# Kernel optimization log

Hardware: AMD Instinct MI355X
Metric: run time of the kernel (lower is better)

The kernel has to match this reference:

```python
import jax, jax.numpy as jnp
import numpy as np

B, N, C = 8, 3136, 128
NUM_HEADS = 2
HEAD_DIM = C // NUM_HEADS  # 64
SCALE = HEAD_DIM ** -0.5


def setup_inputs() -> dict:
    key = jax.random.key(0)
    ks = jax.random.split(key, 10)
    s = 0.02
    return {
        "x": jax.random.normal(ks[0], (B, N, C), jnp.float32),
        "H": 56,
        "W": 56,
        "relative_pos": jax.random.normal(ks[1], (NUM_HEADS, N, N), jnp.float32),
        "Wq": jax.random.normal(ks[2], (C, C), jnp.float32) * s,
        "bq": jnp.zeros((C,), jnp.float32),
        "Wk": jax.random.normal(ks[3], (C, C), jnp.float32) * s,
        "bk": jnp.zeros((C,), jnp.float32),
        "Wv": jax.random.normal(ks[4], (C, C), jnp.float32) * s,
        "bv": jnp.zeros((C,), jnp.float32),
        "Wp": jax.random.normal(ks[5], (C, C), jnp.float32) * s,
        "bp": jnp.zeros((C,), jnp.float32),
    }


def reference(x, H, W, relative_pos, Wq, bq, Wk, bk, Wv, bv, Wp, bp):
    # x: [B, N, C]; sr_ratio == 1 path of Attention.forward
    b, n, c = x.shape
    h, dh = NUM_HEADS, HEAD_DIM
    # q/k/v projections -> [B, h, N, dh] (torch Linear: x @ W.T + b)
    q = (x @ Wq.T + bq).reshape(b, n, h, dh).transpose(0, 2, 1, 3)
    k = (x @ Wk.T + bk).reshape(b, n, h, dh).transpose(0, 2, 1, 3)
    v = (x @ Wv.T + bv).reshape(b, n, h, dh).transpose(0, 2, 1, 3)
    # scores with additive relative-position bias: [B, h, N, N]
    attn = jnp.einsum("bhnd,bhmd->bhnm", q, k) * SCALE + relative_pos[None]
    attn = jax.nn.softmax(attn, axis=-1)
    # AV -> [B, N, C]
    out = jnp.einsum("bhnm,bhmd->bhnd", attn, v).transpose(0, 2, 1, 3).reshape(b, n, c)
    return out @ Wp.T + bp
```

## Files before the change

kernel.cpp:

```cpp
#include <hip/hip_runtime.h>
#include <hip/hip_fp16.h>

#define N_TOK 3136
#define DH 64
#define NHEAD 2
#define CDIM 128
#define BATCH 8
#define NT 49
#define QT1 49
#define MTILES ((BATCH * N_TOK) / 64)
#define EXPBLKS (NHEAD * NT * (N_TOK / 64))
#define QK_SCALE 0.18033688011112f
#define LOG2E 1.4426950408889634f

typedef __attribute__((ext_vector_type(8))) short bf16x8;
typedef __attribute__((ext_vector_type(8))) _Float16 f16x8;
typedef __attribute__((ext_vector_type(2))) _Float16 f16x2;
typedef __attribute__((ext_vector_type(2))) __fp16 fp16x2;
typedef __attribute__((ext_vector_type(4))) float f32x4;
typedef __attribute__((ext_vector_type(16))) float f32x16;
typedef __attribute__((ext_vector_type(4))) unsigned short u16x4;
typedef __attribute__((ext_vector_type(4))) unsigned int u32x4;

__device__ __forceinline__ unsigned short f2bf(float f) {
  unsigned int u = __float_as_uint(f);
  u += 0x7fffu + ((u >> 16) & 1u);
  return (unsigned short)(u >> 16);
}

#define MFMA16(a, b, c)    __builtin_amdgcn_mfma_f32_16x16x32_bf16(a, b, c, 0, 0, 0)
#define MFMA32_BF(a, b, c) __builtin_amdgcn_mfma_f32_32x32x16_bf16(a, b, c, 0, 0, 0)
#define MFMA32_F16(a, b, c) __builtin_amdgcn_mfma_f32_32x32x16_f16(a, b, c, 0, 0, 0)

__device__ __forceinline__ void plswap(unsigned& a, unsigned& b) {
  asm volatile("v_permlane32_swap_b32 %0, %1" : "+v"(a), "+v"(b));
}

__device__ __forceinline__ f16x2 pkrtz(float a, float b) {
  union { fp16x2 p; f16x2 h; } cv;
  cv.p = __builtin_amdgcn_cvt_pkrtz(a, b);
  return cv.h;
}

__device__ __forceinline__ float dot2acc(f16x2 pr, float acc) {
#if __has_builtin(__builtin_amdgcn_fdot2)
  union { f16x2 h; fp16x2 p; } c; c.h = pr;
  fp16x2 ones = {(__fp16)1.0f, (__fp16)1.0f};
  return __builtin_amdgcn_fdot2(c.p, ones, acc, false);
#else
  return acc + (float)pr[0] + (float)pr[1];
#endif
}

__device__ __forceinline__ void stage_w(const float* __restrict__ W,
                                        unsigned short (*wsh)[136], int tid) {
  const float4* Wv4 = (const float4*)W;
#pragma unroll
  for (int i = 0; i < 16; ++i) {
    int f = tid + i * 256;
    float4 v = Wv4[f];
    int row = f >> 5, col = (f & 31) << 2;
    u16x4 pk = { f2bf(v.x), f2bf(v.y), f2bf(v.z), f2bf(v.w) };
    *(u16x4*)&wsh[row][col] = pk;
  }
}

__device__ __forceinline__ void mfma_block(const unsigned short (*xs)[136],
                                           const unsigned short (*wsh)[136],
                                           int w, int lk, int lg, f32x4* acc) {
#pragma unroll
  for (int nf = 0; nf < 8; ++nf) acc[nf] = (f32x4){0.f, 0.f, 0.f, 0.f};
#pragma unroll
  for (int kk = 0; kk < 4; ++kk) {
    bf16x8 a = *(const bf16x8*)&xs[w * 16 + lk][kk * 32 + 8 * lg];
#pragma unroll
    for (int nf = 0; nf < 8; ++nf) {
      bf16x8 b = *(const bf16x8*)&wsh[nf * 16 + lk][kk * 32 + 8 * lg];
      acc[nf] = MFMA16(a, b, acc[nf]);
    }
  }
}

__global__ __launch_bounds__(256)
void pre_kernel(const float* __restrict__ x,
                const float* __restrict__ Wq, const float* __restrict__ bq,
                const float* __restrict__ Wk, const float* __restrict__ bk,
                const float* __restrict__ Wv, const float* __restrict__ bv,
                unsigned short* __restrict__ qo, unsigned short* __restrict__ ko,
                unsigned short* __restrict__ vo,
                const float* __restrict__ rp, __half* __restrict__ E)
{
  __shared__ __align__(16) unsigned short xs[64][136];
  __shared__ __align__(16) unsigned short wsh[128][136];
  const int tid = threadIdx.x;

  if (blockIdx.x >= MTILES) {
    const int eb = blockIdx.x - MTILES;
    const int hkt = eb % (NHEAD * NT);
    const int q0 = (eb / (NHEAD * NT)) * 64;
    const int h = hkt / NT, kt = hkt % NT;
    const int kp = tid & 63;
    const int qi = tid >> 6;

    const int ct = kp >> 5;
    const int kpp = kp & 31;
    const int hi = (kpp >> 2) & 1;
    const int r = (kpp & 3) + ((kpp >> 3) << 2);
    const int didx = hi * 32 + ct * 16 + r;

    const float* src = rp + ((size_t)h * N_TOK + q0) * N_TOK + kt * 64 + kp;
    __half* dst = E + (((size_t)h * NT + kt) * N_TOK + q0) * 64 + didx;
#pragma unroll
    for (int i = 0; i < 16; ++i) {
      int q = qi * 16 + i;
      float v = __expf(src[(size_t)q * N_TOK]);
      dst[(size_t)q * 64] = __float2half(v);
    }
    return;
  }

  const int m0 = blockIdx.x * 64;
  const int w = tid >> 6, l = tid & 63;
  const int lk = l & 15, lg = l >> 4;

  {
    const float4* Xv = (const float4*)(x + (size_t)m0 * CDIM);
#pragma unroll
    for (int i = 0; i < 8; ++i) {
      int f = tid + i * 256;
      float4 v = Xv[f];
      int row = f >> 5, col = (f & 31) << 2;
      u16x4 pk = { f2bf(v.x), f2bf(v.y), f2bf(v.z), f2bf(v.w) };
      *(u16x4*)&xs[row][col] = pk;
    }
  }
  stage_w(Wq, wsh, tid);
  __syncthreads();

  f32x4 acc[8];

  mfma_block(xs, wsh, w, lk, lg, acc);
#pragma unroll
  for (int reg = 0; reg < 4; ++reg) {
    int row = m0 + w * 16 + 4 * lg + reg;
    int bb = row / N_TOK, tok = row - bb * N_TOK;
#pragma unroll
    for (int nf = 0; nf < 8; ++nf) {
      int col = nf * 16 + lk;
      float val = (acc[nf][reg] + bq[col]) * QK_SCALE;
      qo[((size_t)(bb * NHEAD + (nf >> 2)) * N_TOK + tok) * DH + (col & 63)] = f2bf(val);
    }
  }
  __syncthreads();

  stage_w(Wk, wsh, tid);
  __syncthreads();
  mfma_block(xs, wsh, w, lk, lg, acc);
#pragma unroll
  for (int reg = 0; reg < 4; ++reg) {
    int row = m0 + w * 16 + 4 * lg + reg;
    int bb = row / N_TOK, tok = row - bb * N_TOK;
#pragma unroll
    for (int nf = 0; nf < 8; ++nf) {
      int col = nf * 16 + lk;
      float val = acc[nf][reg] + bk[col];
      ko[((size_t)(bb * NHEAD + (nf >> 2)) * N_TOK + tok) * DH + (col & 63)] = f2bf(val);
    }
  }
  __syncthreads();

  stage_w(Wv, wsh, tid);
  __syncthreads();
  mfma_block(xs, wsh, w, lk, lg, acc);
#pragma unroll
  for (int reg = 0; reg < 4; ++reg) {
    int row = m0 + w * 16 + 4 * lg + reg;
    int bb = row / N_TOK, tok = row - bb * N_TOK;
#pragma unroll
    for (int nf = 0; nf < 8; ++nf) {
      int col = nf * 16 + lk;
      float val = acc[nf][reg] + bv[col];
      size_t idx = ((size_t)(bb * NHEAD + (nf >> 2)) * DH + (col & 63)) * N_TOK + tok;
      vo[idx] = __half_as_ushort(__float2half(val));
    }
  }
}

__global__ __launch_bounds__(128)
void attn32(const unsigned short* __restrict__ q_ws,
            const unsigned short* __restrict__ k_ws,
            const unsigned short* __restrict__ v_ws,
            const __half* __restrict__ E,
            unsigned short* __restrict__ attn_out)
{
  __shared__ __align__(16) unsigned short LDSU[2][9216];

  const int b = blockIdx.x, qt = blockIdx.y, head = blockIdx.z;
  const int tid = threadIdx.x;
  const int w = tid >> 6, l = tid & 63;
  const int lq = l & 31, hi = l >> 5;

  const size_t bh = ((size_t)b * NHEAD + head) * N_TOK;
  const unsigned short* Kp = k_ws + bh * DH;
  const _Float16* Vt = (const _Float16*)v_ws + bh * DH;

  const int qg = qt * 64 + w * 32 + lq;

  bf16x8 qf[4];
  {
    const unsigned short* qrow = q_ws + (bh + (size_t)qg) * DH + 8 * hi;
#pragma unroll
    for (int ks = 0; ks < 4; ++ks) qf[ks] = *(const bf16x8*)(qrow + 16 * ks);
  }

  const int sr = tid >> 3, su = tid & 7;
  const int kofs = sr * 72 + su * 8;
  const int gk = sr * DH + su * 8;
  const int gvt = sr * N_TOK + su * 8;

  const __half* Eb = E + (((size_t)head * NT) * N_TOK + (size_t)qg) * DH + hi * 32;

  float lsum = 0.f;
  f32x16 o0, o1;
#pragma unroll
  for (int i = 0; i < 16; ++i) { o0[i] = 0.f; o1[i] = 0.f; }

  bf16x8 kpre[4]; f16x8 vpre[4];
#pragma unroll
  for (int i = 0; i < 4; ++i) {
    kpre[i] = *(const bf16x8*)(Kp + gk + i * 16 * DH);
    vpre[i] = *(const f16x8*)(Vt + gvt + i * 16 * N_TOK);
  }

  u32x4 EwA[4], EwB[4];
  {
    const u32x4* ep = (const u32x4*)Eb;
#pragma unroll
    for (int f = 0; f < 4; ++f) EwA[f] = ep[f];
  }

#pragma unroll
  for (int i = 0; i < 4; ++i) {
    *(bf16x8*)&LDSU[0][kofs + i * 1152] = kpre[i];
    *(f16x8*)&LDSU[0][4608 + kofs + i * 1152] = vpre[i];
  }
  {
    const unsigned short* kn = Kp + (size_t)64 * DH;
    const _Float16* vn = Vt + 64;
#pragma unroll
    for (int i = 0; i < 4; ++i) {
      kpre[i] = *(const bf16x8*)(kn + gk + i * 16 * DH);
      vpre[i] = *(const f16x8*)(vn + gvt + i * 16 * N_TOK);
    }
  }
  asm volatile("s_waitcnt lgkmcnt(0)" ::: "memory");
  __builtin_amdgcn_s_barrier();
  asm volatile("" ::: "memory");

#define ATTN_BODY(PH, KT, EW_CUR, EW_NXT)                                     \
  {                                                                           \
    const bool hasNext = (KT) + 1 < NT;                                       \
    const unsigned short* Kb = &LDSU[PH][0];                                  \
    const unsigned short* Vb = &LDSU[PH][4608];                               \
    unsigned short* Kn = &LDSU[PH ^ 1][0];                                    \
    unsigned short* Vn = &LDSU[PH ^ 1][4608];                                 \
    if (hasNext) {                                         \
      const u32x4* ep = (const u32x4*)(Eb + (size_t)((KT) + 1) * (N_TOK * DH)); \
      _Pragma("unroll") for (int f = 0; f < 4; ++f) EW_NXT[f] = ep[f];        \
    }                                                                         \
                                                           \
    f32x16 s0, s1;                                                            \
    _Pragma("unroll") for (int i = 0; i < 16; ++i) { s0[i] = 0.f; s1[i] = 0.f; } \
    __builtin_amdgcn_s_setprio(1);                                            \
    _Pragma("unroll") for (int ks = 0; ks < 4; ++ks) {                        \
      bf16x8 kf0 = *(const bf16x8*)&Kb[lq * 72 + 16 * ks + 8 * hi];           \
      s0 = MFMA32_BF(kf0, qf[ks], s0);                                        \
      bf16x8 kf1 = *(const bf16x8*)&Kb[(32 + lq) * 72 + 16 * ks + 8 * hi];    \
      s1 = MFMA32_BF(kf1, qf[ks], s1);                                        \
    }                                                                         \
    __builtin_amdgcn_s_setprio(0);                                            \
    if (hasNext) {            \
      _Pragma("unroll") for (int i = 0; i < 4; ++i) {                         \
        *(bf16x8*)&Kn[kofs + i * 1152] = kpre[i];                             \
        *(f16x8*)&Vn[kofs + i * 1152] = vpre[i];                              \
      }                                                                       \
      if ((KT) + 2 < NT) {                                                    \
        const unsigned short* kn2 = Kp + (size_t)((KT) + 2) * 64 * DH;        \
        const _Float16* vn2 = Vt + (size_t)((KT) + 2) * 64;                   \
        _Pragma("unroll") for (int i = 0; i < 4; ++i) {                       \
          kpre[i] = *(const bf16x8*)(kn2 + gk + i * 16 * DH);                 \
          vpre[i] = *(const f16x8*)(vn2 + gvt + i * 16 * N_TOK);              \
        }                                                                     \
      }                                                                       \
    }                                                                         \
                                \
    unsigned pw[16];                                                          \
    _Pragma("unroll") for (int f = 0; f < 4; ++f) {                           \
      int rb = (f & 1) * 8;                                                   \
      _Pragma("unroll") for (int i = 0; i < 4; ++i) {                         \
        float a = (f >> 1) ? s1[rb + 2 * i] : s0[rb + 2 * i];                 \
        float c = (f >> 1) ? s1[rb + 2 * i + 1] : s0[rb + 2 * i + 1];         \
        f16x2 pp = pkrtz(__builtin_amdgcn_exp2f(a), __builtin_amdgcn_exp2f(c)); \
        union { unsigned u; f16x2 h; } ec; ec.u = EW_CUR[f][i];               \
        f16x2 pr = pp * ec.h;                                                 \
        lsum = dot2acc(pr, lsum);                                             \
        union { f16x2 h; unsigned u; } pu; pu.h = pr;                         \
        pw[4 * f + i] = pu.u;                                                 \
      }                                                                       \
      plswap(pw[4 * f + 0], pw[4 * f + 2]);                                   \
      plswap(pw[4 * f + 1], pw[4 * f + 3]);                                   \
    }                                                                         \
                                                        \
    __builtin_amdgcn_s_setprio(1);                                            \
    _Pragma("unroll") for (int ks = 0; ks < 4; ++ks) {                        \
      union { unsigned u[4]; f16x8 v; } pf;                                   \
      _Pragma("unroll") for (int i = 0; i < 4; ++i) pf.u[i] = pw[4 * ks + i]; \
      f16x8 vf0 = *(const f16x8*)&Vb[lq * 72 + 16 * ks + 8 * hi];             \
      o0 = MFMA32_F16(vf0, pf.v, o0);                                         \
      f16x8 vf1 = *(const f16x8*)&Vb[(32 + lq) * 72 + 16 * ks + 8 * hi];      \
      o1 = MFMA32_F16(vf1, pf.v, o1);                                         \
    }                                                                         \
    __builtin_amdgcn_s_setprio(0);                                            \
    if (hasNext) {                                                            \
      asm volatile("s_waitcnt lgkmcnt(0)" ::: "memory");                      \
      __builtin_amdgcn_s_barrier();                                           \
      asm volatile("" ::: "memory");                                          \
    }                                                                         \
  }

  for (int kt2 = 0; kt2 < (NT - 1) / 2; ++kt2) {
    int kt = 2 * kt2;
    ATTN_BODY(0, kt, EwA, EwB);
    ATTN_BODY(1, kt + 1, EwB, EwA);
  }
  ATTN_BODY(0, NT - 1, EwA, EwB);
#undef ATTN_BODY

  lsum += __shfl_xor(lsum, 32, 64);
  float inv = 1.f / lsum;

  __syncthreads();
  unsigned short* Ot = &LDSU[0][0];
  const int orow = (w * 32 + lq) * 72;
#pragma unroll
  for (int dt = 0; dt < 2; ++dt) {
#pragma unroll
    for (int j = 0; j < 8; ++j) {
      float v0 = (dt ? o1[2 * j] : o0[2 * j]) * inv;
      float v1 = (dt ? o1[2 * j + 1] : o0[2 * j + 1]) * inv;
      unsigned pk;
      asm("v_cvt_pk_bf16_f32 %0, %1, %2" : "=v"(pk) : "v"(v0), "v"(v1));
      int d = ((2 * j) & 3) + 8 * ((2 * j) >> 2) + 4 * hi + 32 * dt;
      *(unsigned*)&Ot[orow + d] = pk;
    }
  }
  __syncthreads();
#pragma unroll
  for (int i = 0; i < 4; ++i) {
    int c = tid + 128 * i;
    int ql = c >> 3, du = c & 7;
    int tok = qt * 64 + ql;
    u32x4 val = *(const u32x4*)&Ot[ql * 72 + du * 8];
    *(u32x4*)&attn_out[((size_t)b * N_TOK + tok) * CDIM + head * DH + du * 8] = val;
  }
}

template<bool IN_F32, int OMODE>
__global__ __launch_bounds__(256)
void proj_gemm(const void* __restrict__ Ain, const float* __restrict__ W,
               const float* __restrict__ bias, void* __restrict__ Out,
               float out_scale)
{
  __shared__ __align__(16) unsigned short xs[64][136];
  __shared__ __align__(16) unsigned short wsh[128][136];
  const int tid = threadIdx.x;
  const int m0 = blockIdx.x * 64;
  const int w = tid >> 6, l = tid & 63;
  const int lk = l & 15, lg = l >> 4;

  stage_w(W, wsh, tid);
  if (IN_F32) {
    const float4* Xv = (const float4*)((const float*)Ain + (size_t)m0 * CDIM);
#pragma unroll
    for (int i = 0; i < 8; ++i) {
      int f = tid + i * 256;
      float4 v = Xv[f];
      int row = f >> 5, col = (f & 31) << 2;
      u16x4 pk = { f2bf(v.x), f2bf(v.y), f2bf(v.z), f2bf(v.w) };
      *(u16x4*)&xs[row][col] = pk;
    }
  } else {
    const bf16x8* Xv = (const bf16x8*)((const unsigned short*)Ain + (size_t)m0 * CDIM);
#pragma unroll
    for (int i = 0; i < 4; ++i) {
      int c = tid + i * 256;
      bf16x8 v = Xv[c];
      int row = c >> 4, col = (c & 15) << 3;
      *(bf16x8*)&xs[row][col] = v;
    }
  }
  __syncthreads();

  f32x4 acc[8];
  mfma_block(xs, wsh, w, lk, lg, acc);

#pragma unroll
  for (int reg = 0; reg < 4; ++reg) {
    int row = m0 + w * 16 + 4 * lg + reg;
    int bb = row / N_TOK;
    int tok = row - bb * N_TOK;
#pragma unroll
    for (int nf = 0; nf < 8; ++nf) {
      int col = nf * 16 + lk;
      float val = (acc[nf][reg] + bias[col]) * out_scale;
      if (OMODE == 0) {
        ((float*)Out)[(size_t)row * CDIM + col] = val;
      } else {
        int head = nf >> 2;
        int d = col & 63;
        size_t idx = ((size_t)(bb * NHEAD + head) * N_TOK + tok) * DH + d;
        ((unsigned short*)Out)[idx] = f2bf(val);
      }
    }
  }
}

__global__ __launch_bounds__(256)
void attn_fallback(const unsigned short* __restrict__ q_ws,
                   const unsigned short* __restrict__ k_ws,
                   const unsigned short* __restrict__ v_ws,
                   const float* __restrict__ relpos,
                   unsigned short* __restrict__ attn_out)
{
  __shared__ __align__(16) unsigned short Ks[64][72];
  __shared__ __align__(16) unsigned short Vts[64][72];
  __shared__ __align__(16) unsigned short Ps[4][16][72];

  const int b = blockIdx.x, qt = blockIdx.y, head = blockIdx.z;
  const int tid = threadIdx.x;
  const int w = tid >> 6, l = tid & 63;
  const int lk = l & 15, lg = l >> 4;

  const size_t bh = ((size_t)b * NHEAD + head) * N_TOK;
  const unsigned short* Qp = q_ws + (bh + (size_t)qt * 64) * DH;
  const unsigned short* Kp = k_ws + bh * DH;
  const unsigned short* Vg = v_ws + bh * DH;

  bf16x8 qf0, qf1;
  {
    const unsigned short* qrow = Qp + (size_t)(w * 16 + lk) * DH + 8 * lg;
    qf0 = *(const bf16x8*)qrow;
    qf1 = *(const bf16x8*)(qrow + 32);
  }

  const int kr0 = tid >> 3;
  const int ku = (tid & 7) << 3;
  const int gk0 = kr0 * DH + ku;
  const int gk1 = gk0 + 32 * DH;
  const int vkey = tid & 63;
  const int vd0 = (tid >> 6) << 3;
  const int gv0 = vkey * DH + vd0;
  const int gv1 = gv0 + 32;

  const int qrow0 = qt * 64 + w * 16;
  const float* rpb = relpos + (size_t)head * N_TOK * N_TOK +
                     (size_t)(qrow0 + 4 * lg) * N_TOK + lk;

  float l_run[4] = {0.f, 0.f, 0.f, 0.f};
  f32x4 acc[4];
#pragma unroll
  for (int nf = 0; nf < 4; ++nf) acc[nf] = (f32x4){0.f, 0.f, 0.f, 0.f};

  bf16x8 kpreA = *(const bf16x8*)(Kp + gk0);
  bf16x8 kpreB = *(const bf16x8*)(Kp + gk1);
  bf16x8 vpreA = *(const bf16x8*)(Vg + gv0);
  bf16x8 vpreB = *(const bf16x8*)(Vg + gv1);

  for (int kt = 0; kt < NT; ++kt) {
    float rp[4][4];
#pragma unroll
    for (int r = 0; r < 4; ++r)
#pragma unroll
      for (int ct = 0; ct < 4; ++ct)
        rp[ct][r] = rpb[(size_t)r * N_TOK + kt * 64 + ct * 16];

    asm volatile("s_waitcnt lgkmcnt(0)" ::: "memory");
    __builtin_amdgcn_s_barrier();
    asm volatile("" ::: "memory");

    *(bf16x8*)&Ks[kr0][ku] = kpreA;
    *(bf16x8*)&Ks[kr0 + 32][ku] = kpreB;
#pragma unroll
    for (int j = 0; j < 8; ++j) Vts[vd0 + j][vkey] = ((const unsigned short*)&vpreA)[j];
#pragma unroll
    for (int j = 0; j < 8; ++j) Vts[vd0 + 32 + j][vkey] = ((const unsigned short*)&vpreB)[j];

    if (kt + 1 < NT) {
      const unsigned short* kn = Kp + (size_t)(kt + 1) * 64 * DH;
      const unsigned short* vn = Vg + (size_t)(kt + 1) * 64 * DH;
      kpreA = *(const bf16x8*)(kn + gk0);
      kpreB = *(const bf16x8*)(kn + gk1);
      vpreA = *(const bf16x8*)(vn + gv0);
      vpreB = *(const bf16x8*)(vn + gv1);
    }

    asm volatile("s_waitcnt lgkmcnt(0)" ::: "memory");
    __builtin_amdgcn_s_barrier();
    asm volatile("" ::: "memory");

    f32x4 s[4];
#pragma unroll
    for (int ct = 0; ct < 4; ++ct) s[ct] = (f32x4){0.f, 0.f, 0.f, 0.f};
#pragma unroll
    for (int ct = 0; ct < 4; ++ct) {
      bf16x8 kb0 = *(const bf16x8*)&Ks[ct * 16 + lk][8 * lg];
      s[ct] = MFMA16(qf0, kb0, s[ct]);
      bf16x8 kb1 = *(const bf16x8*)&Ks[ct * 16 + lk][32 + 8 * lg];
      s[ct] = MFMA16(qf1, kb1, s[ct]);
    }

#pragma unroll
    for (int ct = 0; ct < 4; ++ct) {
      float p0 = __builtin_amdgcn_exp2f(fmaf(rp[ct][0], LOG2E, s[ct][0]));
      float p1 = __builtin_amdgcn_exp2f(fmaf(rp[ct][1], LOG2E, s[ct][1]));
      float p2 = __builtin_amdgcn_exp2f(fmaf(rp[ct][2], LOG2E, s[ct][2]));
      float p3 = __builtin_amdgcn_exp2f(fmaf(rp[ct][3], LOG2E, s[ct][3]));
      l_run[0] += p0; l_run[1] += p1; l_run[2] += p2; l_run[3] += p3;
      Ps[w][4 * lg + 0][ct * 16 + lk] = f2bf(p0);
      Ps[w][4 * lg + 1][ct * 16 + lk] = f2bf(p1);
      Ps[w][4 * lg + 2][ct * 16 + lk] = f2bf(p2);
      Ps[w][4 * lg + 3][ct * 16 + lk] = f2bf(p3);
    }

    bf16x8 pa0 = *(const bf16x8*)&Ps[w][lk][8 * lg];
    bf16x8 pa1 = *(const bf16x8*)&Ps[w][lk][32 + 8 * lg];
#pragma unroll
    for (int nf = 0; nf < 4; ++nf) {
      bf16x8 vb0 = *(const bf16x8*)&Vts[nf * 16 + lk][8 * lg];
      acc[nf] = MFMA16(pa0, vb0, acc[nf]);
      bf16x8 vb1 = *(const bf16x8*)&Vts[nf * 16 + lk][32 + 8 * lg];
      acc[nf] = MFMA16(pa1, vb1, acc[nf]);
    }
  }

#pragma unroll
  for (int m = 1; m <= 8; m <<= 1)
#pragma unroll
    for (int r = 0; r < 4; ++r)
      l_run[r] += __shfl_xor(l_run[r], m, 64);

#pragma unroll
  for (int r = 0; r < 4; ++r) {
    int tok = qrow0 + 4 * lg + r;
    float inv = 1.f / l_run[r];
#pragma unroll
    for (int nf = 0; nf < 4; ++nf) {
      attn_out[((size_t)b * N_TOK + tok) * CDIM + head * DH + nf * 16 + lk] =
          f2bf(acc[nf][r] * inv);
    }
  }
}

extern "C" void kernel_launch(void* const* d_in, const int* in_sizes, int n_in,
                              void* d_out, int out_size, void* d_ws, size_t ws_size,
                              hipStream_t stream) {
  (void)in_sizes; (void)n_in; (void)out_size;
  const float* x      = (const float*)d_in[0];
  const float* relpos = (const float*)d_in[3];
  const float* Wq = (const float*)d_in[4];  const float* bq = (const float*)d_in[5];
  const float* Wk = (const float*)d_in[6];  const float* bk = (const float*)d_in[7];
  const float* Wv = (const float*)d_in[8];  const float* bv = (const float*)d_in[9];
  const float* Wp = (const float*)d_in[10]; const float* bp = (const float*)d_in[11];

  const size_t QKV_ELEMS = (size_t)BATCH * NHEAD * N_TOK * DH;
  const size_t E_ELEMS   = (size_t)NHEAD * NT * N_TOK * DH;

  unsigned short* q_ws  = (unsigned short*)d_ws;
  unsigned short* k_ws  = q_ws + QKV_ELEMS;
  unsigned short* v_ws  = k_ws + QKV_ELEMS;
  unsigned short* ao_ws = v_ws + QKV_ELEMS;
  __half* E_ws = (__half*)(ao_ws + QKV_ELEMS);

  const size_t need_mid = (4 * QKV_ELEMS + E_ELEMS) * sizeof(unsigned short);

  dim3 blk(256);

  if (ws_size >= need_mid) {
    pre_kernel<<<MTILES + EXPBLKS, blk, 0, stream>>>(
        x, Wq, bq, Wk, bk, Wv, bv, q_ws, k_ws, v_ws, relpos, (__half*)E_ws);
    attn32<<<dim3(BATCH, QT1, NHEAD), dim3(128), 0, stream>>>(
        q_ws, k_ws, v_ws, (const __half*)E_ws, ao_ws);
  } else {
    proj_gemm<true, 1><<<MTILES, blk, 0, stream>>>((const void*)x, Wq, bq, (void*)q_ws, QK_SCALE);
    proj_gemm<true, 1><<<MTILES, blk, 0, stream>>>((const void*)x, Wk, bk, (void*)k_ws, 1.f);
    proj_gemm<true, 1><<<MTILES, blk, 0, stream>>>((const void*)x, Wv, bv, (void*)v_ws, 1.f);
    attn_fallback<<<dim3(BATCH, N_TOK / 64, NHEAD), blk, 0, stream>>>(
        q_ws, k_ws, v_ws, relpos, ao_ws);
  }

  proj_gemm<false, 0><<<MTILES, blk, 0, stream>>>((const void*)ao_ws, Wp, bp, d_out, 1.f);
}
```

Before: 117.9 us.

## Widen attention blocks to 128 queries and software-pipeline QK^T ahead of softmax

```diff
diff --git a/kernel.cpp b/kernel.cpp
--- a/kernel.cpp
+++ b/kernel.cpp
@@ -7,7 +7,6 @@
 #define CDIM 128
 #define BATCH 8
 #define NT 49
-#define QT1 49
 #define MTILES ((BATCH * N_TOK) / 64)
 #define EXPBLKS (NHEAD * NT * (N_TOK / 64))
 #define QK_SCALE 0.18033688011112f
@@ -186,14 +185,17 @@
   }
 }
 
-__global__ __launch_bounds__(128)
+__global__ __launch_bounds__(256)
 void attn32(const unsigned short* __restrict__ q_ws,
             const unsigned short* __restrict__ k_ws,
             const unsigned short* __restrict__ v_ws,
             const __half* __restrict__ E,
             unsigned short* __restrict__ attn_out)
 {
-  __shared__ __align__(16) unsigned short LDSU[2][9216];
+  __shared__ __align__(16) unsigned short LDSU[27648];
+
+#define KBUF(i) (&LDSU[(i) * 4608])
+#define VBUF(i) (&LDSU[9216 + (i) * 4608])
 
   const int b = blockIdx.x, qt = blockIdx.y, head = blockIdx.z;
   const int tid = threadIdx.x;
@@ -204,7 +206,8 @@
   const unsigned short* Kp = k_ws + bh * DH;
   const _Float16* Vt = (const _Float16*)v_ws + bh * DH;
 
-  const int qg = qt * 64 + w * 32 + lq;
+  int qg = qt * 128 + w * 32 + lq;
+  if (qg > N_TOK - 1) qg = N_TOK - 1;
 
   bf16x8 qf[4];
   {
@@ -215,132 +218,172 @@
 
   const int sr = tid >> 3, su = tid & 7;
   const int kofs = sr * 72 + su * 8;
-  const int gk = sr * DH + su * 8;
-  const int gvt = sr * N_TOK + su * 8;
+  const int gk0 = sr * DH + su * 8, gk1 = gk0 + 32 * DH;
+  const int gvt0 = sr * N_TOK + su * 8, gvt1 = gvt0 + 32 * N_TOK;
 
   const __half* Eb = E + (((size_t)head * NT) * N_TOK + (size_t)qg) * DH + hi * 32;
 
-  float lsum = 0.f;
-  f32x16 o0, o1;
+  float lsum0 = 0.f, lsum1 = 0.f;
+  f32x16 o0, o1, sA0, sA1, sB0, sB1;
 #pragma unroll
   for (int i = 0; i < 16; ++i) { o0[i] = 0.f; o1[i] = 0.f; }
 
-  bf16x8 kpre[4]; f16x8 vpre[4];
-#pragma unroll
-  for (int i = 0; i < 4; ++i) {
-    kpre[i] = *(const bf16x8*)(Kp + gk + i * 16 * DH);
-    vpre[i] = *(const f16x8*)(Vt + gvt + i * 16 * N_TOK);
-  }
+  bf16x8 kpreA = *(const bf16x8*)(Kp + gk0);
+  bf16x8 kpreB = *(const bf16x8*)(Kp + gk1);
+  f16x8 vpreA = *(const f16x8*)(Vt + gvt0);
+  f16x8 vpreB = *(const f16x8*)(Vt + gvt1);
 
   u32x4 EwA[4], EwB[4];
   {
     const u32x4* ep = (const u32x4*)Eb;
 #pragma unroll
     for (int f = 0; f < 4; ++f) EwA[f] = ep[f];
-  }
-
-#pragma unroll
-  for (int i = 0; i < 4; ++i) {
-    *(bf16x8*)&LDSU[0][kofs + i * 1152] = kpre[i];
-    *(f16x8*)&LDSU[0][4608 + kofs + i * 1152] = vpre[i];
-  }
+    const u32x4* ep1 = (const u32x4*)(Eb + (size_t)(N_TOK * DH));
+#pragma unroll
+    for (int f = 0; f < 4; ++f) EwB[f] = ep1[f];
+  }
+
+  *(bf16x8*)&KBUF(0)[kofs] = kpreA;
+  *(bf16x8*)&KBUF(0)[kofs + 32 * 72] = kpreB;
+  *(f16x8*)&VBUF(0)[kofs] = vpreA;
+  *(f16x8*)&VBUF(0)[kofs + 32 * 72] = vpreB;
   {
     const unsigned short* kn = Kp + (size_t)64 * DH;
     const _Float16* vn = Vt + 64;
-#pragma unroll
-    for (int i = 0; i < 4; ++i) {
-      kpre[i] = *(const bf16x8*)(kn + gk + i * 16 * DH);
-      vpre[i] = *(const f16x8*)(vn + gvt + i * 16 * N_TOK);
-    }
+    kpreA = *(const bf16x8*)(kn + gk0);
+    kpreB = *(const bf16x8*)(kn + gk1);
+    vpreA = *(const f16x8*)(vn + gvt0);
+    vpreB = *(const f16x8*)(vn + gvt1);
   }
   asm volatile("s_waitcnt lgkmcnt(0)" ::: "memory");
   __builtin_amdgcn_s_barrier();
   asm volatile("" ::: "memory");
 
-#define ATTN_BODY(PH, KT, EW_CUR, EW_NXT)                                     \
+#pragma unroll
+  for (int i = 0; i < 16; ++i) { sA0[i] = 0.f; sA1[i] = 0.f; }
+  __builtin_amdgcn_s_setprio(1);
+#pragma unroll
+  for (int ks = 0; ks < 4; ++ks) {
+    bf16x8 kf0 = *(const bf16x8*)&KBUF(0)[lq * 72 + 16 * ks + 8 * hi];
+    sA0 = MFMA32_BF(kf0, qf[ks], sA0);
+    bf16x8 kf1 = *(const bf16x8*)&KBUF(0)[(32 + lq) * 72 + 16 * ks + 8 * hi];
+    sA1 = MFMA32_BF(kf1, qf[ks], sA1);
+  }
+  __builtin_amdgcn_s_setprio(0);
+  *(bf16x8*)&KBUF(1)[kofs] = kpreA;
+  *(bf16x8*)&KBUF(1)[kofs + 32 * 72] = kpreB;
+  *(f16x8*)&VBUF(1)[kofs] = vpreA;
+  *(f16x8*)&VBUF(1)[kofs + 32 * 72] = vpreB;
+  {
+    const unsigned short* kn = Kp + (size_t)2 * 64 * DH;
+    const _Float16* vn = Vt + 2 * 64;
+    kpreA = *(const bf16x8*)(kn + gk0);
+    kpreB = *(const bf16x8*)(kn + gk1);
+    vpreA = *(const f16x8*)(vn + gvt0);
+    vpreB = *(const f16x8*)(vn + gvt1);
+  }
+  asm volatile("s_waitcnt lgkmcnt(0)" ::: "memory");
+  __builtin_amdgcn_s_barrier();
+  asm volatile("" ::: "memory");
+
+#define SOFTMAX(S0, S1, EW, PW, LSUM)                                         \
+    _Pragma("unroll") for (int f = 0; f < 4; ++f) {                           \
+      int rb = (f & 1) * 8;                                                   \
+      _Pragma("unroll") for (int i = 0; i < 4; ++i) {                         \
+        float a = (f >> 1) ? S1[rb + 2 * i] : S0[rb + 2 * i];                 \
+        float c = (f >> 1) ? S1[rb + 2 * i + 1] : S0[rb + 2 * i + 1];         \
+        f16x2 pp = pkrtz(__builtin_amdgcn_exp2f(a), __builtin_amdgcn_exp2f(c)); \
+        union { unsigned u; f16x2 h; } ec; ec.u = EW[f][i];                   \
+        f16x2 pr = pp * ec.h;                                                 \
+        LSUM = dot2acc(pr, LSUM);                                             \
+        union { f16x2 h; unsigned u; } pu; pu.h = pr;                         \
+        PW[4 * f + i] = pu.u;                                                 \
+      }                                                                       \
+      plswap(PW[4 * f + 0], PW[4 * f + 2]);                                   \
+      plswap(PW[4 * f + 1], PW[4 * f + 3]);                                   \
+    }
+
+#define BODY(KT, KC, KN, VP, VS, EWC, EWN, SC0, SC1, SP0, SP1, LSUM)          \
   {                                                                           \
-    const bool hasNext = (KT) + 1 < NT;                                       \
-    const unsigned short* Kb = &LDSU[PH][0];                                  \
-    const unsigned short* Vb = &LDSU[PH][4608];                               \
-    unsigned short* Kn = &LDSU[PH ^ 1][0];                                    \
-    unsigned short* Vn = &LDSU[PH ^ 1][4608];                                 \
-    if (hasNext) {                                         \
-      const u32x4* ep = (const u32x4*)(Eb + (size_t)((KT) + 1) * (N_TOK * DH)); \
-      _Pragma("unroll") for (int f = 0; f < 4; ++f) EW_NXT[f] = ep[f];        \
-    }                                                                         \
-                                                           \
-    f32x16 s0, s1;                                                            \
-    _Pragma("unroll") for (int i = 0; i < 16; ++i) { s0[i] = 0.f; s1[i] = 0.f; } \
+                      \
+    _Pragma("unroll") for (int i = 0; i < 16; ++i) { SC0[i] = 0.f; SC1[i] = 0.f; } \
     __builtin_amdgcn_s_setprio(1);                                            \
     _Pragma("unroll") for (int ks = 0; ks < 4; ++ks) {                        \
-      bf16x8 kf0 = *(const bf16x8*)&Kb[lq * 72 + 16 * ks + 8 * hi];           \
-      s0 = MFMA32_BF(kf0, qf[ks], s0);                                        \
-      bf16x8 kf1 = *(const bf16x8*)&Kb[(32 + lq) * 72 + 16 * ks + 8 * hi];    \
-      s1 = MFMA32_BF(kf1, qf[ks], s1);                                        \
+      bf16x8 kf0 = *(const bf16x8*)&(KC)[lq * 72 + 16 * ks + 8 * hi];         \
+      SC0 = MFMA32_BF(kf0, qf[ks], SC0);                                      \
+      bf16x8 kf1 = *(const bf16x8*)&(KC)[(32 + lq) * 72 + 16 * ks + 8 * hi];  \
+      SC1 = MFMA32_BF(kf1, qf[ks], SC1);                                      \
     }                                                                         \
     __builtin_amdgcn_s_setprio(0);                                            \
-    if (hasNext) {            \
-      _Pragma("unroll") for (int i = 0; i < 4; ++i) {                         \
-        *(bf16x8*)&Kn[kofs + i * 1152] = kpre[i];                             \
-        *(f16x8*)&Vn[kofs + i * 1152] = vpre[i];                              \
-      }                                                                       \
+    if ((KT) < NT - 1) {               \
+      *(bf16x8*)&(KN)[kofs] = kpreA;                                          \
+      *(bf16x8*)&(KN)[kofs + 32 * 72] = kpreB;                                \
+      *(f16x8*)&(VS)[kofs] = vpreA;                                           \
+      *(f16x8*)&(VS)[kofs + 32 * 72] = vpreB;                                 \
       if ((KT) + 2 < NT) {                                                    \
         const unsigned short* kn2 = Kp + (size_t)((KT) + 2) * 64 * DH;        \
         const _Float16* vn2 = Vt + (size_t)((KT) + 2) * 64;                   \
-        _Pragma("unroll") for (int i = 0; i < 4; ++i) {                       \
-          kpre[i] = *(const bf16x8*)(kn2 + gk + i * 16 * DH);                 \
-          vpre[i] = *(const f16x8*)(vn2 + gvt + i * 16 * N_TOK);              \
-        }                                                                     \
+        kpreA = *(const bf16x8*)(kn2 + gk0);                                  \
+        kpreB = *(const bf16x8*)(kn2 + gk1);                                  \
+        vpreA = *(const f16x8*)(vn2 + gvt0);                                  \
+        vpreB = *(const f16x8*)(vn2 + gvt1);                                  \
       }                                                                       \
     }                                                                         \
-                                \
+                       \
     unsigned pw[16];                                                          \
-    _Pragma("unroll") for (int f = 0; f < 4; ++f) {                           \
-      int rb = (f & 1) * 8;                                                   \
-      _Pragma("unroll") for (int i = 0; i < 4; ++i) {                         \
-        float a = (f >> 1) ? s1[rb + 2 * i] : s0[rb + 2 * i];                 \
-        float c = (f >> 1) ? s1[rb + 2 * i + 1] : s0[rb + 2 * i + 1];         \
-        f16x2 pp = pkrtz(__builtin_amdgcn_exp2f(a), __builtin_amdgcn_exp2f(c)); \
-        union { unsigned u; f16x2 h; } ec; ec.u = EW_CUR[f][i];               \
-        f16x2 pr = pp * ec.h;                                                 \
-        lsum = dot2acc(pr, lsum);                                             \
-        union { f16x2 h; unsigned u; } pu; pu.h = pr;                         \
-        pw[4 * f + i] = pu.u;                                                 \
-      }                                                                       \
-      plswap(pw[4 * f + 0], pw[4 * f + 2]);                                   \
-      plswap(pw[4 * f + 1], pw[4 * f + 3]);                                   \
+    SOFTMAX(SP0, SP1, EWC, pw, LSUM)                                          \
+    if ((KT) + 1 < NT) {                                                      \
+      const u32x4* ep = (const u32x4*)(Eb + (size_t)((KT) + 1) * (N_TOK * DH)); \
+      _Pragma("unroll") for (int f = 0; f < 4; ++f) EWN[f] = ep[f];           \
     }                                                                         \
-                                                        \
     __builtin_amdgcn_s_setprio(1);                                            \
     _Pragma("unroll") for (int ks = 0; ks < 4; ++ks) {                        \
       union { unsigned u[4]; f16x8 v; } pf;                                   \
       _Pragma("unroll") for (int i = 0; i < 4; ++i) pf.u[i] = pw[4 * ks + i]; \
-      f16x8 vf0 = *(const f16x8*)&Vb[lq * 72 + 16 * ks + 8 * hi];             \
+      f16x8 vf0 = *(const f16x8*)&(VP)[lq * 72 + 16 * ks + 8 * hi];           \
       o0 = MFMA32_F16(vf0, pf.v, o0);                                         \
-      f16x8 vf1 = *(const f16x8*)&Vb[(32 + lq) * 72 + 16 * ks + 8 * hi];      \
+      f16x8 vf1 = *(const f16x8*)&(VP)[(32 + lq) * 72 + 16 * ks + 8 * hi];    \
       o1 = MFMA32_F16(vf1, pf.v, o1);                                         \
     }                                                                         \
     __builtin_amdgcn_s_setprio(0);                                            \
-    if (hasNext) {                                                            \
+    if ((KT) < NT - 1) {                                                      \
       asm volatile("s_waitcnt lgkmcnt(0)" ::: "memory");                      \
       __builtin_amdgcn_s_barrier();                                           \
       asm volatile("" ::: "memory");                                          \
     }                                                                         \
   }
 
-  for (int kt2 = 0; kt2 < (NT - 1) / 2; ++kt2) {
-    int kt = 2 * kt2;
-    ATTN_BODY(0, kt, EwA, EwB);
-    ATTN_BODY(1, kt + 1, EwB, EwA);
-  }
-  ATTN_BODY(0, NT - 1, EwA, EwB);
-#undef ATTN_BODY
-
+  for (int j = 0; j < 12; ++j) {
+    int kt = 1 + 4 * j;
+    BODY(kt,     KBUF(1), KBUF(0), VBUF(0), VBUF(2), EwA, EwA, sB0, sB1, sA0, sA1, lsum0);
+    BODY(kt + 1, KBUF(0), KBUF(1), VBUF(1), VBUF(3), EwB, EwB, sA0, sA1, sB0, sB1, lsum1);
+    BODY(kt + 2, KBUF(1), KBUF(0), VBUF(2), VBUF(0), EwA, EwA, sB0, sB1, sA0, sA1, lsum0);
+    BODY(kt + 3, KBUF(0), KBUF(1), VBUF(3), VBUF(1), EwB, EwB, sA0, sA1, sB0, sB1, lsum1);
+  }
+#undef BODY
+
+  {
+    unsigned pw[16];
+    SOFTMAX(sA0, sA1, EwA, pw, lsum0)
+#pragma unroll
+    for (int ks = 0; ks < 4; ++ks) {
+      union { unsigned u[4]; f16x8 v; } pf;
+#pragma unroll
+      for (int i = 0; i < 4; ++i) pf.u[i] = pw[4 * ks + i];
+      f16x8 vf0 = *(const f16x8*)&VBUF(0)[lq * 72 + 16 * ks + 8 * hi];
+      o0 = MFMA32_F16(vf0, pf.v, o0);
+      f16x8 vf1 = *(const f16x8*)&VBUF(0)[(32 + lq) * 72 + 16 * ks + 8 * hi];
+      o1 = MFMA32_F16(vf1, pf.v, o1);
+    }
+  }
+#undef SOFTMAX
+
+  float lsum = lsum0 + lsum1;
   lsum += __shfl_xor(lsum, 32, 64);
   float inv = 1.f / lsum;
 
   __syncthreads();
-  unsigned short* Ot = &LDSU[0][0];
+  unsigned short* Ot = &LDSU[0];
   const int orow = (w * 32 + lq) * 72;
 #pragma unroll
   for (int dt = 0; dt < 2; ++dt) {
@@ -357,12 +400,16 @@
   __syncthreads();
 #pragma unroll
   for (int i = 0; i < 4; ++i) {
-    int c = tid + 128 * i;
+    int c = tid + 256 * i;
     int ql = c >> 3, du = c & 7;
-    int tok = qt * 64 + ql;
-    u32x4 val = *(const u32x4*)&Ot[ql * 72 + du * 8];
-    *(u32x4*)&attn_out[((size_t)b * N_TOK + tok) * CDIM + head * DH + du * 8] = val;
-  }
+    int tok = qt * 128 + ql;
+    if (tok < N_TOK) {
+      u32x4 val = *(const u32x4*)&Ot[ql * 72 + du * 8];
+      *(u32x4*)&attn_out[((size_t)b * N_TOK + tok) * CDIM + head * DH + du * 8] = val;
+    }
+  }
+#undef KBUF
+#undef VBUF
 }
 
 template<bool IN_F32, int OMODE>
@@ -588,7 +635,7 @@
   if (ws_size >= need_mid) {
     pre_kernel<<<MTILES + EXPBLKS, blk, 0, stream>>>(
         x, Wq, bq, Wk, bk, Wv, bv, q_ws, k_ws, v_ws, relpos, (__half*)E_ws);
-    attn32<<<dim3(BATCH, QT1, NHEAD), dim3(128), 0, stream>>>(
+    attn32<<<dim3(BATCH, (N_TOK + 127) / 128, NHEAD), blk, 0, stream>>>(
         q_ws, k_ws, v_ws, (const __half*)E_ws, ao_ws);
   } else {
     proj_gemm<true, 1><<<MTILES, blk, 0, stream>>>((const void*)x, Wq, bq, (void*)q_ws, QK_SCALE);
```

After: 122.9 us. +4.2%, slower.
